# Kernel optimization log

Hardware: AMD Instinct MI355X
Metric: run time of the kernel (lower is better)

The kernel has to match this reference:

```python
import jax, jax.numpy as jnp
import numpy as np

N_NODES = 1_000_000
N_EDGES = 16_000_000


def setup_inputs() -> dict:
    key = jax.random.key(0)
    ks = jax.random.split(key, 12)
    feat = jax.random.normal(ks[0], (N_NODES, 1), dtype=jnp.float32)
    # symmetric GCN norm D^{-1/2}; positive values in (0, 1]
    norm = jax.random.uniform(ks[1], (N_NODES, 1), dtype=jnp.float32, minval=0.05, maxval=1.0)
    src = jax.random.randint(ks[2], (N_EDGES,), 0, N_NODES, dtype=jnp.int32)
    dst = jax.random.randint(ks[3], (N_EDGES,), 0, N_NODES, dtype=jnp.int32)
    dims = [(1, 3), (3, 3), (3, 3), (3, 3), (3, 3), (3, 1)]
    params = {}
    for i, (fi, fo) in enumerate(dims):
        w = jax.random.normal(ks[4 + i], (fi, fo), dtype=jnp.float32) * (1.0 / np.sqrt(fi))
        params[f"W{i+1}"] = w
        params[f"b{i+1}"] = jnp.zeros((fo,), dtype=jnp.float32)
    return dict(feat=feat, norm=norm, src=src, dst=dst, **params)


def _gcn_layer(h, norm, W, b, src, dst, n_nodes):
    # DGL-style GraphConv with symmetric norm:
    #   h = h * norm; agg_i = sum_{(j->i) in E} h_j; h = agg * norm; h = h @ W + b; relu
    h = h * norm                                   # [N, F]
    msgs = jnp.take(h, src, axis=0)                # [E, F] irregular gather
    agg = jax.ops.segment_sum(msgs, dst, num_segments=n_nodes)  # [N, F] scatter-add
    agg = agg * norm
    return jax.nn.relu(agg @ W + b)


def reference(feat, norm, W1, b1, W2, b2, W3, b3, W4, b4, W5, b5, W6, b6, src, dst):
    n = feat.shape[0]
    h = feat
    for W, b in ((W1, b1), (W2, b2), (W3, b3), (W4, b4), (W5, b5), (W6, b6)):
        h = _gcn_layer(h, norm, W, b, src, dst, n)
    return h  # [N, 1]
```

## Files before the change

kernel.cpp:

```cpp
#include <hip/hip_runtime.h>


#define BT 256
#define NBLK 256
#define BSHIFT 9
#define BSIZE 512
#define LMASK 511
#define NBKT 2048

__global__ void k_init(const float* __restrict__ feat, const float* __restrict__ norm,
                       float* __restrict__ s0, int N) {
  int i = blockIdx.x * BT + threadIdx.x;
  if (i < N) s0[i] = feat[i] * norm[i];
}

__global__ void k_phist(const int* __restrict__ dst, int* __restrict__ histB,
                        int E, int chunk) {
  __shared__ int h[NBKT];
  for (int i = threadIdx.x; i < NBKT; i += BT) h[i] = 0;
  __syncthreads();
  int b = blockIdx.x;
  int beg = b * chunk, end = min(beg + chunk, E);
  for (int i = beg + threadIdx.x; i < end; i += BT)
    atomicAdd(&h[dst[i] >> BSHIFT], 1);
  __syncthreads();
  for (int k = threadIdx.x; k < NBKT; k += BT)
    histB[b * NBKT + k] = h[k];
}

__global__ void k_transp(const int* __restrict__ in, int* __restrict__ out, int R, int C) {
  __shared__ int tile[64][65];
  int c0 = blockIdx.x * 64, r0 = blockIdx.y * 64;
  int tx = threadIdx.x & 63, ty = threadIdx.x >> 6;
  for (int j = 0; j < 16; ++j) {
    int r = ty + j * 4;
    tile[r][tx] = in[(r0 + r) * C + c0 + tx];
  }
  __syncthreads();
  for (int j = 0; j < 16; ++j) {
    int r = ty + j * 4;
    out[(c0 + r) * R + r0 + tx] = tile[tx][r];
  }
}

__global__ void k_blockSum(const int* __restrict__ data, int* __restrict__ partial, int M) {
  __shared__ int tmp[BT];
  int i = blockIdx.x * BT + threadIdx.x;
  tmp[threadIdx.x] = (i < M) ? data[i] : 0;
  __syncthreads();
  for (int off = BT / 2; off > 0; off >>= 1) {
    if (threadIdx.x < off) tmp[threadIdx.x] += tmp[threadIdx.x + off];
    __syncthreads();
  }
  if (threadIdx.x == 0) partial[blockIdx.x] = tmp[0];
}

__global__ void k_scanPartials(int* __restrict__ partial, int nb) {
  __shared__ int tmp[BT];
  __shared__ int carry;
  int t = threadIdx.x;
  if (t == 0) carry = 0;
  __syncthreads();
  for (int base = 0; base < nb; base += BT) {
    int i = base + t;
    int v = (i < nb) ? partial[i] : 0;
    tmp[t] = v;
    __syncthreads();
    for (int off = 1; off < BT; off <<= 1) {
      int x = 0;
      if (t >= off) x = tmp[t - off];
      __syncthreads();
      tmp[t] += x;
      __syncthreads();
    }
    if (i < nb) partial[i] = tmp[t] - v + carry;
    __syncthreads();
    if (t == BT - 1) carry += tmp[BT - 1];
    __syncthreads();
  }
}

__global__ void k_scanFinal(int* __restrict__ data, const int* __restrict__ partial, int M) {
  __shared__ int tmp[BT];
  int t = threadIdx.x;
  int i = blockIdx.x * BT + t;
  int v = (i < M) ? data[i] : 0;
  tmp[t] = v;
  __syncthreads();
  for (int off = 1; off < BT; off <<= 1) {
    int x = 0;
    if (t >= off) x = tmp[t - off];
    __syncthreads();
    tmp[t] += x;
    __syncthreads();
  }
  if (i < M) data[i] = tmp[t] - v + partial[blockIdx.x];
}

__global__ void k_pscatter(const int* __restrict__ src, const int* __restrict__ dst,
                           const int* __restrict__ scanT, unsigned int* __restrict__ packed,
                           int E, int chunk) {
  __shared__ int cur[NBKT];
  int b = blockIdx.x;
  for (int k = threadIdx.x; k < NBKT; k += BT) cur[k] = scanT[b * NBKT + k];
  __syncthreads();
  int beg = b * chunk, end = min(beg + chunk, E);
  for (int i = beg + threadIdx.x; i < end; i += BT) {
    int s = src[i], d = dst[i];
    int pos = atomicAdd(&cur[d >> BSHIFT], 1);
    packed[pos] = ((unsigned)s << BSHIFT) | (unsigned)(d & LMASK);
  }
}

__global__ void k_layer1(const int* __restrict__ scanT, const unsigned int* __restrict__ packed,
                         const float* __restrict__ s0, const float* __restrict__ norm,
                         const float* __restrict__ W1, const float* __restrict__ b1,
                         float* __restrict__ sNext, int N) {
  __shared__ float a[BSIZE];
  int k = blockIdx.x;
  for (int i = threadIdx.x; i < BSIZE; i += BT) a[i] = 0.0f;
  int beg = scanT[k], end = scanT[k + 1];
  __syncthreads();
  for (int e = beg + threadIdx.x; e < end; e += BT) {
    unsigned p = packed[e];
    atomicAdd(&a[p & LMASK], s0[p >> BSHIFT]);
  }
  __syncthreads();
  int node0 = k << BSHIFT;
  for (int t = threadIdx.x; t < BSIZE; t += BT) {
    int node = node0 + t;
    if (node >= N) break;
    float n = norm[node];
    float pre = a[t] * n;
    float h0 = fmaxf(0.0f, pre * W1[0] + b1[0]);
    float h1 = fmaxf(0.0f, pre * W1[1] + b1[1]);
    float h2 = fmaxf(0.0f, pre * W1[2] + b1[2]);
    ((float4*)sNext)[node] = make_float4(h0 * n, h1 * n, h2 * n, 0.0f);
  }
}

__global__ void k_layer3(const int* __restrict__ scanT, const unsigned int* __restrict__ packed,
                         const float* __restrict__ sPrev, const float* __restrict__ norm,
                         const float* __restrict__ W, const float* __restrict__ bias,
                         float* __restrict__ sNext, int N) {
  __shared__ float a0[BSIZE], a1[BSIZE], a2[BSIZE];
  int k = blockIdx.x;
  for (int i = threadIdx.x; i < BSIZE; i += BT) { a0[i] = 0.0f; a1[i] = 0.0f; a2[i] = 0.0f; }
  int beg = scanT[k], end = scanT[k + 1];
  __syncthreads();
  for (int e = beg + threadIdx.x; e < end; e += BT) {
    unsigned p = packed[e];
    int loc = p & LMASK;
    float4 m = ((const float4*)sPrev)[p >> BSHIFT];
    atomicAdd(&a0[loc], m.x);
    atomicAdd(&a1[loc], m.y);
    atomicAdd(&a2[loc], m.z);
  }
  __syncthreads();
  int node0 = k << BSHIFT;
  for (int t = threadIdx.x; t < BSIZE; t += BT) {
    int node = node0 + t;
    if (node >= N) break;
    float n = norm[node];
    float x0 = a0[t] * n, x1 = a1[t] * n, x2 = a2[t] * n;
    float h0 = fmaxf(0.0f, x0 * W[0] + x1 * W[3] + x2 * W[6] + bias[0]);
    float h1 = fmaxf(0.0f, x0 * W[1] + x1 * W[4] + x2 * W[7] + bias[1]);
    float h2 = fmaxf(0.0f, x0 * W[2] + x1 * W[5] + x2 * W[8] + bias[2]);
    ((float4*)sNext)[node] = make_float4(h0 * n, h1 * n, h2 * n, 0.0f);
  }
}

__global__ void k_layer5(const int* __restrict__ scanT, const unsigned int* __restrict__ packed,
                         const float* __restrict__ sPrev, const float* __restrict__ norm,
                         const float* __restrict__ W5, const float* __restrict__ b5,
                         const float* __restrict__ W6, float* __restrict__ sB, int N) {
  __shared__ float a0[BSIZE], a1[BSIZE], a2[BSIZE];
  int k = blockIdx.x;
  for (int i = threadIdx.x; i < BSIZE; i += BT) { a0[i] = 0.0f; a1[i] = 0.0f; a2[i] = 0.0f; }
  int beg = scanT[k], end = scanT[k + 1];
  __syncthreads();
  for (int e = beg + threadIdx.x; e < end; e += BT) {
    unsigned p = packed[e];
    int loc = p & LMASK;
    float4 m = ((const float4*)sPrev)[p >> BSHIFT];
    atomicAdd(&a0[loc], m.x);
    atomicAdd(&a1[loc], m.y);
    atomicAdd(&a2[loc], m.z);
  }
  __syncthreads();
  int node0 = k << BSHIFT;
  for (int t = threadIdx.x; t < BSIZE; t += BT) {
    int node = node0 + t;
    if (node >= N) break;
    float n = norm[node];
    float x0 = a0[t] * n, x1 = a1[t] * n, x2 = a2[t] * n;
    float h0 = fmaxf(0.0f, x0 * W5[0] + x1 * W5[3] + x2 * W5[6] + b5[0]);
    float h1 = fmaxf(0.0f, x0 * W5[1] + x1 * W5[4] + x2 * W5[7] + b5[1]);
    float h2 = fmaxf(0.0f, x0 * W5[2] + x1 * W5[5] + x2 * W5[8] + b5[2]);
    sB[node] = (h0 * W6[0] + h1 * W6[1] + h2 * W6[2]) * n;
  }
}

__global__ void k_layer6(const int* __restrict__ scanT, const unsigned int* __restrict__ packed,
                         const float* __restrict__ sB, const float* __restrict__ norm,
                         const float* __restrict__ b6, float* __restrict__ out, int N) {
  __shared__ float a[BSIZE];
  int k = blockIdx.x;
  for (int i = threadIdx.x; i < BSIZE; i += BT) a[i] = 0.0f;
  int beg = scanT[k], end = scanT[k + 1];
  __syncthreads();
  for (int e = beg + threadIdx.x; e < end; e += BT) {
    unsigned p = packed[e];
    atomicAdd(&a[p & LMASK], sB[p >> BSHIFT]);
  }
  __syncthreads();
  int node0 = k << BSHIFT;
  for (int t = threadIdx.x; t < BSIZE; t += BT) {
    int node = node0 + t;
    if (node >= N) break;
    out[node] = fmaxf(0.0f, a[t] * norm[node] + b6[0]);
  }
}

extern "C" void kernel_launch(void* const* d_in, const int* in_sizes, int n_in,
                              void* d_out, int out_size, void* d_ws, size_t ws_size,
                              hipStream_t stream) {
  const float* feat = (const float*)d_in[0];
  const float* norm = (const float*)d_in[1];
  const int* src = (const int*)d_in[2];
  const int* dst = (const int*)d_in[3];
  const float* W1 = (const float*)d_in[4];
  const float* b1 = (const float*)d_in[5];
  const float* W2 = (const float*)d_in[6];
  const float* b2 = (const float*)d_in[7];
  const float* W3 = (const float*)d_in[8];
  const float* b3 = (const float*)d_in[9];
  const float* W4 = (const float*)d_in[10];
  const float* b4 = (const float*)d_in[11];
  const float* W5 = (const float*)d_in[12];
  const float* b5 = (const float*)d_in[13];
  const float* W6 = (const float*)d_in[14];
  const float* b6 = (const float*)d_in[15];
  float* out = (float*)d_out;

  const int N = in_sizes[0];
  const int E = in_sizes[2];
  const int nbNode = (N + BT - 1) / BT;
  const int nBkt = (N + BSIZE - 1) >> BSHIFT;
  const int chunk = (E + NBLK - 1) / NBLK;
  const int M = NBKT * NBLK;

  unsigned int* packed = (unsigned int*)d_ws;
  int* histB = (int*)(packed + (size_t)E);
  int* histT = histB + (size_t)M;
  int* scanT = histT + (size_t)M;
  int* partial = scanT + (size_t)M;
  float* s0B = (float*)(partial + M / BT);
  float* sA = s0B + (size_t)N;
  float* sA2 = sA + (size_t)4 * N;

  k_init<<<nbNode, BT, 0, stream>>>(feat, norm, s0B, N);
  k_phist<<<NBLK, BT, 0, stream>>>(dst, histB, E, chunk);
  {
    dim3 g1(NBKT / 64, NBLK / 64);
    k_transp<<<g1, BT, 0, stream>>>(histB, histT, NBLK, NBKT);
  }
  k_blockSum<<<M / BT, BT, 0, stream>>>(histT, partial, M);
  k_scanPartials<<<1, BT, 0, stream>>>(partial, M / BT);
  k_scanFinal<<<M / BT, BT, 0, stream>>>(histT, partial, M);
  {
    dim3 g2(NBLK / 64, NBKT / 64);
    k_transp<<<g2, BT, 0, stream>>>(histT, scanT, NBKT, NBLK);
  }
  k_pscatter<<<NBLK, BT, 0, stream>>>(src, dst, scanT, packed, E, chunk);

  k_layer1<<<nBkt, BT, 0, stream>>>(scanT, packed, s0B, norm, W1, b1, sA, N);
  k_layer3<<<nBkt, BT, 0, stream>>>(scanT, packed, sA, norm, W2, b2, sA2, N);
  k_layer3<<<nBkt, BT, 0, stream>>>(scanT, packed, sA2, norm, W3, b3, sA, N);
  k_layer3<<<nBkt, BT, 0, stream>>>(scanT, packed, sA, norm, W4, b4, sA2, N);
  k_layer5<<<nBkt, BT, 0, stream>>>(scanT, packed, sA2, norm, W5, b5, W6, s0B, N);
  k_layer6<<<nBkt, BT, 0, stream>>>(scanT, packed, s0B, norm, b6, out, N);
}
```

Baseline: 1.810 ms.

## Use coarser 4096-node destination buckets, 1024-thread layer blocks, vectorized edge loads

Bucket granularity grows from 512 to 4096 destination nodes, which cuts the histogram, transpose and scan work to 256 buckets per partition. Layer kernels now run 1024-thread blocks, one per bucket, and read packed edges with uint4 loads, handling an alignment prologue and a tail. The histogram and scatter kernels also use int4 loads of src/dst, with chunk sizes rounded up to a multiple of 4. In exchange, only about 245 large blocks cover the GPU, which may leave CUs underused or unevenly loaded. Each layer3 block also needs 48KB of LDS.

```diff
diff --git a/kernel.cpp b/kernel.cpp
--- a/kernel.cpp
+++ b/kernel.cpp
@@ -3,10 +3,12 @@
 
 #define BT 256
 #define NBLK 256
-#define BSHIFT 9
-#define BSIZE 512
-#define LMASK 511
-#define NBKT 2048
+#define BSHIFT 12
+#define BSIZE 4096
+#define LMASK 4095
+#define NBKT 256
+#define M (NBLK * NBKT)
+#define BTL 1024
 
 __global__ void k_init(const float* __restrict__ feat, const float* __restrict__ norm,
                        float* __restrict__ s0, int N) {
@@ -17,15 +19,21 @@
 __global__ void k_phist(const int* __restrict__ dst, int* __restrict__ histB,
                         int E, int chunk) {
   __shared__ int h[NBKT];
-  for (int i = threadIdx.x; i < NBKT; i += BT) h[i] = 0;
+  if (threadIdx.x < NBKT) h[threadIdx.x] = 0;
   __syncthreads();
   int b = blockIdx.x;
   int beg = b * chunk, end = min(beg + chunk, E);
-  for (int i = beg + threadIdx.x; i < end; i += BT)
-    atomicAdd(&h[dst[i] >> BSHIFT], 1);
-  __syncthreads();
-  for (int k = threadIdx.x; k < NBKT; k += BT)
-    histB[b * NBKT + k] = h[k];
+  int i = beg + (int)threadIdx.x * 4;
+  for (; i + 3 < end; i += BT * 4) {
+    int4 v = *(const int4*)(dst + i);
+    atomicAdd(&h[v.x >> BSHIFT], 1);
+    atomicAdd(&h[v.y >> BSHIFT], 1);
+    atomicAdd(&h[v.z >> BSHIFT], 1);
+    atomicAdd(&h[v.w >> BSHIFT], 1);
+  }
+  for (; i < end; ++i) atomicAdd(&h[dst[i] >> BSHIFT], 1);
+  __syncthreads();
+  if (threadIdx.x < NBKT) histB[b * NBKT + threadIdx.x] = h[threadIdx.x];
 }
 
 __global__ void k_transp(const int* __restrict__ in, int* __restrict__ out, int R, int C) {
@@ -43,10 +51,10 @@
   }
 }
 
-__global__ void k_blockSum(const int* __restrict__ data, int* __restrict__ partial, int M) {
+__global__ void k_blockSum(const int* __restrict__ data, int* __restrict__ partial, int Mlen) {
   __shared__ int tmp[BT];
   int i = blockIdx.x * BT + threadIdx.x;
-  tmp[threadIdx.x] = (i < M) ? data[i] : 0;
+  tmp[threadIdx.x] = (i < Mlen) ? data[i] : 0;
   __syncthreads();
   for (int off = BT / 2; off > 0; off >>= 1) {
     if (threadIdx.x < off) tmp[threadIdx.x] += tmp[threadIdx.x + off];
@@ -80,11 +88,11 @@
   }
 }
 
-__global__ void k_scanFinal(int* __restrict__ data, const int* __restrict__ partial, int M) {
+__global__ void k_scanFinal(int* __restrict__ data, const int* __restrict__ partial, int Mlen) {
   __shared__ int tmp[BT];
   int t = threadIdx.x;
   int i = blockIdx.x * BT + t;
-  int v = (i < M) ? data[i] : 0;
+  int v = (i < Mlen) ? data[i] : 0;
   tmp[t] = v;
   __syncthreads();
   for (int off = 1; off < BT; off <<= 1) {
@@ -94,7 +102,7 @@
     tmp[t] += x;
     __syncthreads();
   }
-  if (i < M) data[i] = tmp[t] - v + partial[blockIdx.x];
+  if (i < Mlen) data[i] = tmp[t] - v + partial[blockIdx.x];
 }
 
 __global__ void k_pscatter(const int* __restrict__ src, const int* __restrict__ dst,
@@ -102,36 +110,72 @@
                            int E, int chunk) {
   __shared__ int cur[NBKT];
   int b = blockIdx.x;
-  for (int k = threadIdx.x; k < NBKT; k += BT) cur[k] = scanT[b * NBKT + k];
+  if (threadIdx.x < NBKT) cur[threadIdx.x] = scanT[b * NBKT + threadIdx.x];
   __syncthreads();
   int beg = b * chunk, end = min(beg + chunk, E);
-  for (int i = beg + threadIdx.x; i < end; i += BT) {
-    int s = src[i], d = dst[i];
-    int pos = atomicAdd(&cur[d >> BSHIFT], 1);
-    packed[pos] = ((unsigned)s << BSHIFT) | (unsigned)(d & LMASK);
-  }
-}
-
-__global__ void k_layer1(const int* __restrict__ scanT, const unsigned int* __restrict__ packed,
-                         const float* __restrict__ s0, const float* __restrict__ norm,
-                         const float* __restrict__ W1, const float* __restrict__ b1,
-                         float* __restrict__ sNext, int N) {
+  int i = beg + (int)threadIdx.x * 4;
+  for (; i + 3 < end; i += BT * 4) {
+    int4 u = *(const int4*)(src + i);
+    int4 v = *(const int4*)(dst + i);
+    int p;
+    p = atomicAdd(&cur[v.x >> BSHIFT], 1);
+    packed[p] = ((unsigned)u.x << BSHIFT) | (unsigned)(v.x & LMASK);
+    p = atomicAdd(&cur[v.y >> BSHIFT], 1);
+    packed[p] = ((unsigned)u.y << BSHIFT) | (unsigned)(v.y & LMASK);
+    p = atomicAdd(&cur[v.z >> BSHIFT], 1);
+    packed[p] = ((unsigned)u.z << BSHIFT) | (unsigned)(v.z & LMASK);
+    p = atomicAdd(&cur[v.w >> BSHIFT], 1);
+    packed[p] = ((unsigned)u.w << BSHIFT) | (unsigned)(v.w & LMASK);
+  }
+  for (; i < end; ++i) {
+    int p = atomicAdd(&cur[dst[i] >> BSHIFT], 1);
+    packed[p] = ((unsigned)src[i] << BSHIFT) | (unsigned)(dst[i] & LMASK);
+  }
+}
+
+
+#define ACC3(p)                                             \
+  {                                                         \
+    unsigned pp = (p);                                      \
+    float4 m = ((const float4*)sPrev)[pp >> BSHIFT];        \
+    int loc = pp & LMASK;                                   \
+    atomicAdd(&a0[loc], m.x);                               \
+    atomicAdd(&a1[loc], m.y);                               \
+    atomicAdd(&a2[loc], m.z);                               \
+  }
+
+#define ACC1(p)                                             \
+  {                                                         \
+    unsigned pp = (p);                                      \
+    atomicAdd(&a[pp & LMASK], sIn[pp >> BSHIFT]);           \
+  }
+
+__global__ __launch_bounds__(BTL) void k_layer1(
+    const int* __restrict__ scanT, const unsigned int* __restrict__ packed,
+    const float* __restrict__ sIn, const float* __restrict__ norm,
+    const float* __restrict__ W1, const float* __restrict__ b1,
+    float* __restrict__ sNext, int N) {
   __shared__ float a[BSIZE];
   int k = blockIdx.x;
-  for (int i = threadIdx.x; i < BSIZE; i += BT) a[i] = 0.0f;
+  for (int i = threadIdx.x; i < BSIZE; i += BTL) a[i] = 0.0f;
   int beg = scanT[k], end = scanT[k + 1];
   __syncthreads();
-  for (int e = beg + threadIdx.x; e < end; e += BT) {
-    unsigned p = packed[e];
-    atomicAdd(&a[p & LMASK], s0[p >> BSHIFT]);
-  }
+  int abeg = min(end, (beg + 3) & ~3);
+  int t = beg + (int)threadIdx.x;
+  if (t < abeg) ACC1(packed[t]);
+  int i = abeg + (int)threadIdx.x * 4;
+  for (; i + 3 < end; i += BTL * 4) {
+    uint4 p4 = *(const uint4*)(packed + i);
+    ACC1(p4.x) ACC1(p4.y) ACC1(p4.z) ACC1(p4.w)
+  }
+  for (; i < end; ++i) ACC1(packed[i]);
   __syncthreads();
   int node0 = k << BSHIFT;
-  for (int t = threadIdx.x; t < BSIZE; t += BT) {
-    int node = node0 + t;
+  for (int tt = threadIdx.x; tt < BSIZE; tt += BTL) {
+    int node = node0 + tt;
     if (node >= N) break;
     float n = norm[node];
-    float pre = a[t] * n;
+    float pre = a[tt] * n;
     float h0 = fmaxf(0.0f, pre * W1[0] + b1[0]);
     float h1 = fmaxf(0.0f, pre * W1[1] + b1[1]);
     float h2 = fmaxf(0.0f, pre * W1[2] + b1[2]);
@@ -139,30 +183,32 @@
   }
 }
 
-__global__ void k_layer3(const int* __restrict__ scanT, const unsigned int* __restrict__ packed,
-                         const float* __restrict__ sPrev, const float* __restrict__ norm,
-                         const float* __restrict__ W, const float* __restrict__ bias,
-                         float* __restrict__ sNext, int N) {
+__global__ __launch_bounds__(BTL) void k_layer3(
+    const int* __restrict__ scanT, const unsigned int* __restrict__ packed,
+    const float* __restrict__ sPrev, const float* __restrict__ norm,
+    const float* __restrict__ W, const float* __restrict__ bias,
+    float* __restrict__ sNext, int N) {
   __shared__ float a0[BSIZE], a1[BSIZE], a2[BSIZE];
   int k = blockIdx.x;
-  for (int i = threadIdx.x; i < BSIZE; i += BT) { a0[i] = 0.0f; a1[i] = 0.0f; a2[i] = 0.0f; }
+  for (int i = threadIdx.x; i < BSIZE; i += BTL) { a0[i] = 0.0f; a1[i] = 0.0f; a2[i] = 0.0f; }
   int beg = scanT[k], end = scanT[k + 1];
   __syncthreads();
-  for (int e = beg + threadIdx.x; e < end; e += BT) {
-    unsigned p = packed[e];
-    int loc = p & LMASK;
-    float4 m = ((const float4*)sPrev)[p >> BSHIFT];
-    atomicAdd(&a0[loc], m.x);
-    atomicAdd(&a1[loc], m.y);
-    atomicAdd(&a2[loc], m.z);
-  }
+  int abeg = min(end, (beg + 3) & ~3);
+  int t = beg + (int)threadIdx.x;
+  if (t < abeg) ACC3(packed[t]);
+  int i = abeg + (int)threadIdx.x * 4;
+  for (; i + 3 < end; i += BTL * 4) {
+    uint4 p4 = *(const uint4*)(packed + i);
+    ACC3(p4.x) ACC3(p4.y) ACC3(p4.z) ACC3(p4.w)
+  }
+  for (; i < end; ++i) ACC3(packed[i]);
   __syncthreads();
   int node0 = k << BSHIFT;
-  for (int t = threadIdx.x; t < BSIZE; t += BT) {
-    int node = node0 + t;
+  for (int tt = threadIdx.x; tt < BSIZE; tt += BTL) {
+    int node = node0 + tt;
     if (node >= N) break;
     float n = norm[node];
-    float x0 = a0[t] * n, x1 = a1[t] * n, x2 = a2[t] * n;
+    float x0 = a0[tt] * n, x1 = a1[tt] * n, x2 = a2[tt] * n;
     float h0 = fmaxf(0.0f, x0 * W[0] + x1 * W[3] + x2 * W[6] + bias[0]);
     float h1 = fmaxf(0.0f, x0 * W[1] + x1 * W[4] + x2 * W[7] + bias[1]);
     float h2 = fmaxf(0.0f, x0 * W[2] + x1 * W[5] + x2 * W[8] + bias[2]);
@@ -170,30 +216,32 @@
   }
 }
 
-__global__ void k_layer5(const int* __restrict__ scanT, const unsigned int* __restrict__ packed,
-                         const float* __restrict__ sPrev, const float* __restrict__ norm,
-                         const float* __restrict__ W5, const float* __restrict__ b5,
-                         const float* __restrict__ W6, float* __restrict__ sB, int N) {
+__global__ __launch_bounds__(BTL) void k_layer5(
+    const int* __restrict__ scanT, const unsigned int* __restrict__ packed,
+    const float* __restrict__ sPrev, const float* __restrict__ norm,
+    const float* __restrict__ W5, const float* __restrict__ b5,
+    const float* __restrict__ W6, float* __restrict__ sB, int N) {
   __shared__ float a0[BSIZE], a1[BSIZE], a2[BSIZE];
   int k = blockIdx.x;
-  for (int i = threadIdx.x; i < BSIZE; i += BT) { a0[i] = 0.0f; a1[i] = 0.0f; a2[i] = 0.0f; }
+  for (int i = threadIdx.x; i < BSIZE; i += BTL) { a0[i] = 0.0f; a1[i] = 0.0f; a2[i] = 0.0f; }
   int beg = scanT[k], end = scanT[k + 1];
   __syncthreads();
-  for (int e = beg + threadIdx.x; e < end; e += BT) {
-    unsigned p = packed[e];
-    int loc = p & LMASK;
-    float4 m = ((const float4*)sPrev)[p >> BSHIFT];
-    atomicAdd(&a0[loc], m.x);
-    atomicAdd(&a1[loc], m.y);
-    atomicAdd(&a2[loc], m.z);
-  }
+  int abeg = min(end, (beg + 3) & ~3);
+  int t = beg + (int)threadIdx.x;
+  if (t < abeg) ACC3(packed[t]);
+  int i = abeg + (int)threadIdx.x * 4;
+  for (; i + 3 < end; i += BTL * 4) {
+    uint4 p4 = *(const uint4*)(packed + i);
+    ACC3(p4.x) ACC3(p4.y) ACC3(p4.z) ACC3(p4.w)
+  }
+  for (; i < end; ++i) ACC3(packed[i]);
   __syncthreads();
   int node0 = k << BSHIFT;
-  for (int t = threadIdx.x; t < BSIZE; t += BT) {
-    int node = node0 + t;
+  for (int tt = threadIdx.x; tt < BSIZE; tt += BTL) {
+    int node = node0 + tt;
     if (node >= N) break;
     float n = norm[node];
-    float x0 = a0[t] * n, x1 = a1[t] * n, x2 = a2[t] * n;
+    float x0 = a0[tt] * n, x1 = a1[tt] * n, x2 = a2[tt] * n;
     float h0 = fmaxf(0.0f, x0 * W5[0] + x1 * W5[3] + x2 * W5[6] + b5[0]);
     float h1 = fmaxf(0.0f, x0 * W5[1] + x1 * W5[4] + x2 * W5[7] + b5[1]);
     float h2 = fmaxf(0.0f, x0 * W5[2] + x1 * W5[5] + x2 * W5[8] + b5[2]);
@@ -201,24 +249,30 @@
   }
 }
 
-__global__ void k_layer6(const int* __restrict__ scanT, const unsigned int* __restrict__ packed,
-                         const float* __restrict__ sB, const float* __restrict__ norm,
-                         const float* __restrict__ b6, float* __restrict__ out, int N) {
+__global__ __launch_bounds__(BTL) void k_layer6(
+    const int* __restrict__ scanT, const unsigned int* __restrict__ packed,
+    const float* __restrict__ sIn, const float* __restrict__ norm,
+    const float* __restrict__ b6, float* __restrict__ out, int N) {
   __shared__ float a[BSIZE];
   int k = blockIdx.x;
-  for (int i = threadIdx.x; i < BSIZE; i += BT) a[i] = 0.0f;
+  for (int i = threadIdx.x; i < BSIZE; i += BTL) a[i] = 0.0f;
   int beg = scanT[k], end = scanT[k + 1];
   __syncthreads();
-  for (int e = beg + threadIdx.x; e < end; e += BT) {
-    unsigned p = packed[e];
-    atomicAdd(&a[p & LMASK], sB[p >> BSHIFT]);
-  }
+  int abeg = min(end, (beg + 3) & ~3);
+  int t = beg + (int)threadIdx.x;
+  if (t < abeg) ACC1(packed[t]);
+  int i = abeg + (int)threadIdx.x * 4;
+  for (; i + 3 < end; i += BTL * 4) {
+    uint4 p4 = *(const uint4*)(packed + i);
+    ACC1(p4.x) ACC1(p4.y) ACC1(p4.z) ACC1(p4.w)
+  }
+  for (; i < end; ++i) ACC1(packed[i]);
   __syncthreads();
   int node0 = k << BSHIFT;
-  for (int t = threadIdx.x; t < BSIZE; t += BT) {
-    int node = node0 + t;
+  for (int tt = threadIdx.x; tt < BSIZE; tt += BTL) {
+    int node = node0 + tt;
     if (node >= N) break;
-    out[node] = fmaxf(0.0f, a[t] * norm[node] + b6[0]);
+    out[node] = fmaxf(0.0f, a[tt] * norm[node] + b6[0]);
   }
 }
 
@@ -247,8 +301,7 @@
   const int E = in_sizes[2];
   const int nbNode = (N + BT - 1) / BT;
   const int nBkt = (N + BSIZE - 1) >> BSHIFT;
-  const int chunk = (E + NBLK - 1) / NBLK;
-  const int M = NBKT * NBLK;
+  const int chunk = (((E + NBLK - 1) / NBLK) + 3) & ~3;
 
   unsigned int* packed = (unsigned int*)d_ws;
   int* histB = (int*)(packed + (size_t)E);
@@ -274,10 +327,10 @@
   }
   k_pscatter<<<NBLK, BT, 0, stream>>>(src, dst, scanT, packed, E, chunk);
 
-  k_layer1<<<nBkt, BT, 0, stream>>>(scanT, packed, s0B, norm, W1, b1, sA, N);
-  k_layer3<<<nBkt, BT, 0, stream>>>(scanT, packed, sA, norm, W2, b2, sA2, N);
-  k_layer3<<<nBkt, BT, 0, stream>>>(scanT, packed, sA2, norm, W3, b3, sA, N);
-  k_layer3<<<nBkt, BT, 0, stream>>>(scanT, packed, sA, norm, W4, b4, sA2, N);
-  k_layer5<<<nBkt, BT, 0, stream>>>(scanT, packed, sA2, norm, W5, b5, W6, s0B, N);
-  k_layer6<<<nBkt, BT, 0, stream>>>(scanT, packed, s0B, norm, b6, out, N);
-}
+  k_layer1<<<nBkt, BTL, 0, stream>>>(scanT, packed, s0B, norm, W1, b1, sA, N);
+  k_layer3<<<nBkt, BTL, 0, stream>>>(scanT, packed, sA, norm, W2, b2, sA2, N);
+  k_layer3<<<nBkt, BTL, 0, stream>>>(scanT, packed, sA2, norm, W3, b3, sA, N);
+  k_layer3<<<nBkt, BTL, 0, stream>>>(scanT, packed, sA, norm, W4, b4, sA2, N);
+  k_layer5<<<nBkt, BTL, 0, stream>>>(scanT, packed, sA2, norm, W5, b5, W6, s0B, N);
+  k_layer6<<<nBkt, BTL, 0, stream>>>(scanT, packed, s0B, norm, b6, out, N);
+}
```

New measurement: 1.556 ms. 1.16x faster.
